# Performance work log

Measured on AMD Instinct MI355X. Metric: run time of the kernel, lower is better.

## Reference

```python
import jax, jax.numpy as jnp
import numpy as np

G = 128   # long_term_attn_g
H = 8     # num_attn_heads


def setup_inputs() -> dict:
    key = jax.random.key(0)
    ks = jax.random.split(key, 8)
    b, d, t, dk = 8, 1024, 8192, 512  # dk = model_dim // 2
    return {
        "qk": jax.random.normal(ks[0], (b, d, t), jnp.float32),
        "masks": jnp.ones((b, 1, t), jnp.float32),
        "wq": jax.random.normal(ks[1], (dk, d), jnp.float32) * 0.02,
        "bq": jnp.zeros((dk,), jnp.float32),
        "wk": jax.random.normal(ks[2], (dk, d), jnp.float32) * 0.02,
        "bk": jnp.zeros((dk,), jnp.float32),
        "wv": jax.random.normal(ks[3], (dk, d), jnp.float32) * 0.02,
        "bv": jnp.zeros((dk,), jnp.float32),
        "wo": jax.random.normal(ks[4], (d, dk), jnp.float32) * 0.02,
        "bo": jnp.zeros((d,), jnp.float32),
    }


def _to_patches(x, g):
    # convert_to_patches + rearrange 'b d np p -> (b p) d np'
    b, d, t = x.shape
    pad = (-t) % g
    x = jnp.pad(x, ((0, 0), (0, 0), (0, pad)))
    npat = x.shape[-1] // g
    return x.reshape(b, d, npat, g).transpose(0, 3, 1, 2).reshape(b * g, d, npat)


def reference(qk, masks, wq, bq, wk, bk, wv, bv, wo, bo):
    b, d, t = qk.shape
    xp = _to_patches(qk, G)     # [(b g), d, npat]  -- q, k, v source
    mp = _to_patches(masks, G)  # [(b g), 1, npat]  -- key-side attention mask

    # pointwise Conv1d projections == per-timestep matmuls
    q = jnp.einsum('od,bdt->bot', wq, xp) + bq[:, None]
    k = jnp.einsum('od,bdt->bot', wk, xp) + bk[:, None]
    v = jnp.einsum('od,bdt->bot', wv, xp) + bv[:, None]

    dk = wq.shape[0]
    dh = dk // H
    bg, _, npat = q.shape
    qh = q.reshape(bg, H, dh, npat)
    kh = k.reshape(bg, H, dh, npat)
    vh = v.reshape(bg, H, dh, npat)

    scores = jnp.einsum('bhdi,bhdj->bhij', qh, kh) / jnp.sqrt(jnp.float32(dh))
    scores = jnp.where(mp[:, :, None, :] > 0, scores, jnp.float32(-1e9))
    attn = jax.nn.softmax(scores, axis=-1)
    out = jnp.einsum('bhij,bhdj->bhdi', attn, vh).reshape(bg, dk, npat)

    # out_proj = GELU -> Conv1d(dk -> model_dim, k=1)
    out = jax.nn.gelu(out, approximate=False)
    out = jnp.einsum('od,bdt->bot', wo, out) + bo[:, None]

    # undo reshape: '(b g) d np -> b d (np g)', trim padding
    out = out.reshape(b, G, d, npat).transpose(0, 2, 3, 1).reshape(b, d, npat * G)[:, :, :t]
    return out * masks
```

## Files before the change

kernel.cpp:

```cpp
#include <hip/hip_runtime.h>
#include <hip/hip_bf16.h>
#include <cmath>

typedef __attribute__((ext_vector_type(4))) float f32x4;
typedef __attribute__((ext_vector_type(8))) short s16x8;

typedef __attribute__((address_space(1))) const void glb_void_t;
typedef __attribute__((address_space(3))) void lds_void_t;

#define MFMA(a, b, c) __builtin_amdgcn_mfma_f32_16x16x32_bf16(a, b, c, 0, 0, 0)
#define GLOAD_LDS(g, l) __builtin_amdgcn_global_load_lds((glb_void_t*)(g), (lds_void_t*)(l), 16, 0, 0)

__device__ __forceinline__ unsigned short bf(float x) {
  union { float f; unsigned u; } c; c.f = x;
  unsigned r = (c.u + 0x7fffu + ((c.u >> 16) & 1u)) >> 16;
  return (unsigned short)r;
}

__global__ void k_prep(const float* __restrict__ wq, const float* __restrict__ wk,
                       const float* __restrict__ wv, const float* __restrict__ bq,
                       const float* __restrict__ bk, const float* __restrict__ bv,
                       const float* __restrict__ wo,
                       __hip_bfloat16* __restrict__ wqkv, __hip_bfloat16* __restrict__ wob,
                       float* __restrict__ bqkv) {
  const int NW = 1536 * 1024, NO = 1024 * 512;
  for (int i = blockIdx.x * blockDim.x + threadIdx.x; i < NW + NO + 1536;
       i += gridDim.x * blockDim.x) {
    if (i < NW) {
      int r = i >> 10;
      float v = (r < 512) ? wq[i] : ((r < 1024) ? wk[i - 512 * 1024] : wv[i - 1024 * 1024]);
      ((unsigned short*)wqkv)[i] = bf(v);
    } else if (i < NW + NO) {
      int j = i - NW;
      ((unsigned short*)wob)[j] = bf(wo[j]);
    } else {
      int j = i - NW - NO;
      bqkv[j] = (j < 512) ? bq[j] : ((j < 1024) ? bk[j - 512] : bv[j - 1024]);
    }
  }
}

__global__ __launch_bounds__(256) void k_transpose(const float* __restrict__ qk,
                                                   __hip_bfloat16* __restrict__ qkT) {
  __shared__ float tile[64][65];
  const int b = blockIdx.z, t0 = blockIdx.x * 64, d0 = blockIdx.y * 64;
  const int tid = threadIdx.x;
  const int tq = tid & 15, dr = tid >> 4;
  const float* src = qk + ((size_t)b * 1024 + d0) * 8192 + t0;
#pragma unroll
  for (int i = 0; i < 4; i++) {
    int d = dr + i * 16;
    float4 v = *(const float4*)(src + (size_t)d * 8192 + tq * 4);
    tile[d][tq * 4 + 0] = v.x; tile[d][tq * 4 + 1] = v.y;
    tile[d][tq * 4 + 2] = v.z; tile[d][tq * 4 + 3] = v.w;
  }
  __syncthreads();
  const int d4 = (tid & 15) * 4, tr = tid >> 4;
  unsigned short* dst = (unsigned short*)qkT + ((size_t)b * 8192 + t0) * 1024 + d0;
#pragma unroll
  for (int i = 0; i < 4; i++) {
    int t = tr + i * 16;
    ushort4 o4;
    o4.x = bf(tile[d4 + 0][t]); o4.y = bf(tile[d4 + 1][t]);
    o4.z = bf(tile[d4 + 2][t]); o4.w = bf(tile[d4 + 3][t]);
    *(ushort4*)(dst + (size_t)t * 1024 + d4) = o4;
  }
}

__device__ __forceinline__ void stage_half(char* lds_base, const char* gbase,
                                           int ktile, int w, int l) {
#pragma unroll
  for (int r = 0; r < 2; ++r) {
    int row = r * 64 + w * 8 + (l >> 3);
    int cb = ((l & 7) * 16) ^ ((row & 7) << 4);
    GLOAD_LDS(gbase + (size_t)row * 2048 + (size_t)ktile * 128 + cb,
              lds_base + (r * 64 + w * 8) * 128);
  }
}

__global__ __launch_bounds__(512, 2) void k_qkv(const __hip_bfloat16* __restrict__ qkT,
                                                const __hip_bfloat16* __restrict__ wqkv,
                                                const float* __restrict__ bqkv,
                                                __hip_bfloat16* __restrict__ qkv) {
  __shared__ char smem[131072];
  const int NT = 16;
  const int b = blockIdx.z, t0 = blockIdx.x * 256, o0 = blockIdx.y * 256;
  const int tid = threadIdx.x, l = tid & 63, w = tid >> 6;
  const int c = l & 15, g = l >> 4;
  const int wm = w >> 2, wn = w & 3;
  const int cbase = (g * 16) ^ ((c & 7) << 4);

  const char* qpanel = (const char*)qkT + ((size_t)b * 8192 + t0) * 2048;
  const char* wpanel = (const char*)wqkv + (size_t)o0 * 2048;

#define STAGE_A(tt, h) stage_half(smem + ((tt)&1) * 32768 + (h) * 16384, \
                                  qpanel + (size_t)(h) * 262144, (tt), w, l)
#define STAGE_B(tt, h) stage_half(smem + 65536 + ((tt)&1) * 32768 + (h) * 16384, \
                                  wpanel + (size_t)(h) * 262144, (tt), w, l)

  f32x4 acc[8][4];
#pragma unroll
  for (int i = 0; i < 8; i++)
#pragma unroll
    for (int j = 0; j < 4; j++) acc[i][j] = (f32x4){0.f, 0.f, 0.f, 0.f};

  STAGE_A(0, 0); STAGE_A(0, 1); STAGE_B(0, 0); STAGE_B(0, 1);
  STAGE_B(1, 0); STAGE_A(1, 0); STAGE_A(1, 1);
  asm volatile("s_waitcnt vmcnt(6)" ::: "memory");
  __builtin_amdgcn_s_barrier();

#pragma unroll 2
  for (int t = 0; t < NT; ++t) {
    const int buf = t & 1;
    const char* Ah = smem + buf * 32768 + wm * 16384;
    const char* Bh = smem + 65536 + buf * 32768 + (wn >> 1) * 16384;
    const int brow = (wn & 1) * 64;
    s16x8 avLo[4][2], avHi[4][2], bv[4][2];

#pragma unroll
    for (int mi = 0; mi < 4; ++mi)
#pragma unroll
      for (int kk = 0; kk < 2; ++kk)
        avLo[mi][kk] = *(const s16x8*)(Ah + (mi * 16 + c) * 128 + (cbase ^ (kk << 6)));
#pragma unroll
    for (int ni = 0; ni < 4; ++ni)
#pragma unroll
      for (int kk = 0; kk < 2; ++kk)
        bv[ni][kk] = *(const s16x8*)(Bh + (brow + ni * 16 + c) * 128 + (cbase ^ (kk << 6)));
    if (t + 1 < NT) STAGE_B(t + 1, 1);
    __builtin_amdgcn_s_barrier();
    asm volatile("s_waitcnt lgkmcnt(0)" ::: "memory");
    __builtin_amdgcn_sched_barrier(0);
    __builtin_amdgcn_s_setprio(1);
#pragma unroll
    for (int mi = 0; mi < 4; ++mi)
#pragma unroll
      for (int ni = 0; ni < 2; ++ni)
#pragma unroll
        for (int kk = 0; kk < 2; ++kk)
          acc[mi][ni] = MFMA(avLo[mi][kk], bv[ni][kk], acc[mi][ni]);
    __builtin_amdgcn_s_setprio(0);
    __builtin_amdgcn_s_barrier();

#pragma unroll
    for (int mi = 0; mi < 4; ++mi)
#pragma unroll
      for (int kk = 0; kk < 2; ++kk)
        avHi[mi][kk] = *(const s16x8*)(Ah + (64 + mi * 16 + c) * 128 + (cbase ^ (kk << 6)));
    if (t + 2 < NT) STAGE_B(t + 2, 0);
    __builtin_amdgcn_s_barrier();
    asm volatile("s_waitcnt lgkmcnt(0)" ::: "memory");
    __builtin_amdgcn_sched_barrier(0);
    __builtin_amdgcn_s_setprio(1);
#pragma unroll
    for (int mi = 0; mi < 4; ++mi)
#pragma unroll
      for (int ni = 0; ni < 2; ++ni)
#pragma unroll
        for (int kk = 0; kk < 2; ++kk)
          acc[mi][ni + 2] = MFMA(avLo[mi][kk], bv[ni + 2][kk], acc[mi][ni + 2]);
    __builtin_amdgcn_s_setprio(0);
    __builtin_amdgcn_s_barrier();

    if (t + 2 < NT) STAGE_A(t + 2, 0);
    __builtin_amdgcn_s_barrier();
    __builtin_amdgcn_s_setprio(1);
#pragma unroll
    for (int mi = 0; mi < 4; ++mi)
#pragma unroll
      for (int ni = 0; ni < 2; ++ni)
#pragma unroll
        for (int kk = 0; kk < 2; ++kk)
          acc[mi + 4][ni] = MFMA(avHi[mi][kk], bv[ni][kk], acc[mi + 4][ni]);
    __builtin_amdgcn_s_setprio(0);
    __builtin_amdgcn_s_barrier();

    if (t + 2 < NT) STAGE_A(t + 2, 1);
    if (t + 2 < NT) {
      asm volatile("s_waitcnt vmcnt(6)" ::: "memory");
    } else {
      asm volatile("s_waitcnt vmcnt(0)" ::: "memory");
    }
    __builtin_amdgcn_s_barrier();
    __builtin_amdgcn_sched_barrier(0);
    __builtin_amdgcn_s_setprio(1);
#pragma unroll
    for (int mi = 0; mi < 4; ++mi)
#pragma unroll
      for (int ni = 0; ni < 2; ++ni)
#pragma unroll
        for (int kk = 0; kk < 2; ++kk)
          acc[mi + 4][ni + 2] = MFMA(avHi[mi][kk], bv[ni + 2][kk], acc[mi + 4][ni + 2]);
    __builtin_amdgcn_s_setprio(0);
    __builtin_amdgcn_s_barrier();
  }
#undef STAGE_A
#undef STAGE_B

  unsigned short* outb = (unsigned short*)qkv + ((size_t)b * 8192 + t0) * 1536 + o0;
  float bias[4];
#pragma unroll
  for (int ni = 0; ni < 4; ni++) bias[ni] = bqkv[o0 + wn * 64 + ni * 16 + c];
#pragma unroll
  for (int mi = 0; mi < 8; mi++)
#pragma unroll
    for (int r = 0; r < 4; r++) {
      int t = wm * 128 + mi * 16 + g * 4 + r;
#pragma unroll
      for (int ni = 0; ni < 4; ni++) {
        int o = wn * 64 + ni * 16 + c;
        outb[(size_t)t * 1536 + o] = bf(acc[mi][ni][r] + bias[ni]);
      }
    }
}

__global__ __launch_bounds__(64) void k_attn(const __hip_bfloat16* __restrict__ qkv,
                                             const float* __restrict__ masks,
                                             __hip_bfloat16* __restrict__ a_out) {
  const int l = threadIdx.x, c = l & 15, g = l >> 4;
  const int h = blockIdx.x & 7, bg = blockIdx.x >> 3;
  const int gg = bg & 127, b = bg >> 7;
  const size_t rowstep = (size_t)128 * 1536;
  const __hip_bfloat16* base = qkv + ((size_t)b * 8192 + gg) * 1536 + h * 64;
  const __hip_bfloat16* Qb = base;
  const __hip_bfloat16* Kb = base + 512;
  const __hip_bfloat16* Vb = base + 1024;

  s16x8 kf[4][2], qf[4][2];
#pragma unroll
  for (int f = 0; f < 4; f++)
#pragma unroll
    for (int kk = 0; kk < 2; kk++) {
      size_t roff = (size_t)(f * 16 + c) * rowstep + kk * 32 + g * 8;
      kf[f][kk] = *(const s16x8*)(Kb + roff);
      qf[f][kk] = *(const s16x8*)(Qb + roff);
    }
  f32x4 st[4][4];
#pragma unroll
  for (int i = 0; i < 4; i++)
#pragma unroll
    for (int j = 0; j < 4; j++) st[i][j] = (f32x4){0.f, 0.f, 0.f, 0.f};
#pragma unroll
  for (int mj = 0; mj < 4; mj++)
#pragma unroll
    for (int ni = 0; ni < 4; ni++)
#pragma unroll
      for (int kk = 0; kk < 2; kk++)
        st[mj][ni] = MFMA(kf[mj][kk], qf[ni][kk], st[mj][ni]);

  float mk[4][4];
#pragma unroll
  for (int mj = 0; mj < 4; mj++)
#pragma unroll
    for (int r = 0; r < 4; r++)
      mk[mj][r] = masks[(size_t)b * 8192 + (size_t)(mj * 16 + g * 4 + r) * 128 + gg];

  float inv[4];
#pragma unroll
  for (int ni = 0; ni < 4; ni++) {
    float m = -1e30f;
#pragma unroll
    for (int mj = 0; mj < 4; mj++)
#pragma unroll
      for (int r = 0; r < 4; r++) {
        float s = st[mj][ni][r] * 0.125f;
        s = (mk[mj][r] > 0.f) ? s : -1e9f;
        st[mj][ni][r] = s;
        m = fmaxf(m, s);
      }
    m = fmaxf(m, __shfl_xor(m, 16));
    m = fmaxf(m, __shfl_xor(m, 32));
    float sm = 0.f;
#pragma unroll
    for (int mj = 0; mj < 4; mj++)
#pragma unroll
      for (int r = 0; r < 4; r++) {
        float p = expf(st[mj][ni][r] - m);
        st[mj][ni][r] = p;
        sm += p;
      }
    sm += __shfl_xor(sm, 16);
    sm += __shfl_xor(sm, 32);
    inv[ni] = 1.f / sm;
  }
#pragma unroll
  for (int mj = 0; mj < 4; mj++)
#pragma unroll
    for (int ni = 0; ni < 4; ni++)
#pragma unroll
      for (int r = 0; r < 4; r++) st[mj][ni][r] *= inv[ni];

  unsigned qd[4][4][2];
#pragma unroll
  for (int ni = 0; ni < 4; ni++)
#pragma unroll
    for (int mj = 0; mj < 4; mj++)
#pragma unroll
      for (int wv = 0; wv < 2; wv++)
        qd[ni][mj][wv] = (unsigned)bf(st[mj][ni][2 * wv]) |
                         ((unsigned)bf(st[mj][ni][2 * wv + 1]) << 16);

  f32x4 oacc[4][4];
#pragma unroll
  for (int i = 0; i < 4; i++)
#pragma unroll
    for (int j = 0; j < 4; j++) oacc[i][j] = (f32x4){0.f, 0.f, 0.f, 0.f};

  const int srcA = c + 32 * (g & 1);
  const int srcB = srcA + 16;
  const bool hi = (g >= 2);
#pragma unroll
  for (int kk = 0; kk < 2; kk++) {
    s16x8 af[4];
#pragma unroll
    for (int ni = 0; ni < 4; ni++) {
      unsigned a0 = __shfl(qd[ni][2 * kk][0], srcA);
      unsigned b0 = __shfl(qd[ni][2 * kk + 1][0], srcA);
      unsigned a1 = __shfl(qd[ni][2 * kk][1], srcA);
      unsigned b1 = __shfl(qd[ni][2 * kk + 1][1], srcA);
      unsigned a2 = __shfl(qd[ni][2 * kk][0], srcB);
      unsigned b2 = __shfl(qd[ni][2 * kk + 1][0], srcB);
      unsigned a3 = __shfl(qd[ni][2 * kk][1], srcB);
      unsigned b3 = __shfl(qd[ni][2 * kk + 1][1], srcB);
      union { unsigned u[4]; s16x8 v; } uu;
      uu.u[0] = hi ? b0 : a0;
      uu.u[1] = hi ? b1 : a1;
      uu.u[2] = hi ? b2 : a2;
      uu.u[3] = hi ? b3 : a3;
      af[ni] = uu.v;
    }
    s16x8 bvv[4];
#pragma unroll
    for (int fd = 0; fd < 4; fd++) {
      s16x8 t;
#pragma unroll
      for (int e = 0; e < 8; e++)
        t[e] = *(const short*)(Vb + (size_t)(kk * 32 + g * 8 + e) * rowstep + fd * 16 + c);
      bvv[fd] = t;
    }
#pragma unroll
    for (int fi = 0; fi < 4; fi++)
#pragma unroll
      for (int fd = 0; fd < 4; fd++)
        oacc[fi][fd] = MFMA(af[fi], bvv[fd], oacc[fi][fd]);
  }

  unsigned short* ob = (unsigned short*)a_out + ((size_t)b * 8192 + gg) * 512 + h * 64;
#pragma unroll
  for (int fi = 0; fi < 4; fi++)
#pragma unroll
    for (int fd = 0; fd < 4; fd++)
#pragma unroll
      for (int r = 0; r < 4; r++) {
        float x = oacc[fi][fd][r];
        float ge = 0.5f * x * (1.f + erff(x * 0.70710678118f));
        int i = fi * 16 + g * 4 + r;
        ob[(size_t)i * (128 * 512) + fd * 16 + c] = bf(ge);
      }
}

__global__ __launch_bounds__(512) void k_out(const __hip_bfloat16* __restrict__ wob,
                                             const __hip_bfloat16* __restrict__ a,
                                             const float* __restrict__ bo,
                                             const float* __restrict__ masks,
                                             float* __restrict__ y) {
  __shared__ char smem[256 * 128 + 128 * 128];
  char* As = smem;
  char* Bs = smem + 32768;
  const int b = blockIdx.z, t0 = blockIdx.x * 128, o0 = blockIdx.y * 256;
  const int tid = threadIdx.x, l = tid & 63, w = tid >> 6;
  const int c = l & 15, g = l >> 4;
  const int wm = w >> 1, wn = w & 1;
  const int lrow = l >> 3, lcol = (l & 7) * 16;

  f32x4 acc[4][4];
#pragma unroll
  for (int i = 0; i < 4; i++)
#pragma unroll
    for (int j = 0; j < 4; j++) acc[i][j] = (f32x4){0.f, 0.f, 0.f, 0.f};

  const char* wbase = (const char*)(wob + (size_t)o0 * 512);
  const char* abase = (const char*)(a + ((size_t)b * 8192 + t0) * 512);

  for (int ks = 0; ks < 8; ks++) {
    __syncthreads();
#pragma unroll
    for (int ii = 0; ii < 4; ii++) {
      int row = w * 32 + ii * 8 + lrow;
      int cb = lcol ^ ((row & 7) << 4);
      const char* gp = wbase + (size_t)row * 1024 + ks * 128 + cb;
      GLOAD_LDS(gp, As + (w * 32 + ii * 8) * 128);
    }
#pragma unroll
    for (int ii = 0; ii < 2; ii++) {
      int row = w * 16 + ii * 8 + lrow;
      int cb = lcol ^ ((row & 7) << 4);
      const char* gp = abase + (size_t)row * 1024 + ks * 128 + cb;
      GLOAD_LDS(gp, Bs + (w * 16 + ii * 8) * 128);
    }
    __syncthreads();
#pragma unroll
    for (int kk = 0; kk < 2; kk++) {
      s16x8 av[4], bv[4];
#pragma unroll
      for (int mi = 0; mi < 4; mi++) {
        int row = wm * 64 + mi * 16 + c;
        int cb = (kk * 64 + g * 16) ^ ((row & 7) << 4);
        av[mi] = *(const s16x8*)(As + row * 128 + cb);
      }
#pragma unroll
      for (int ni = 0; ni < 4; ni++) {
        int row = wn * 64 + ni * 16 + c;
        int cb = (kk * 64 + g * 16) ^ ((row & 7) << 4);
        bv[ni] = *(const s16x8*)(Bs + row * 128 + cb);
      }
#pragma unroll
      for (int mi = 0; mi < 4; mi++)
#pragma unroll
        for (int ni = 0; ni < 4; ni++)
          acc[mi][ni] = MFMA(av[mi], bv[ni], acc[mi][ni]);
    }
  }
  int tcol[4];
  float mk[4];
#pragma unroll
  for (int ni = 0; ni < 4; ni++) {
    tcol[ni] = t0 + wn * 64 + ni * 16 + c;
    mk[ni] = masks[(size_t)b * 8192 + tcol[ni]];
  }
#pragma unroll
  for (int mi = 0; mi < 4; mi++)
#pragma unroll
    for (int r = 0; r < 4; r++) {
      int od = o0 + wm * 64 + mi * 16 + g * 4 + r;
      float bias = bo[od];
      float* yrow = y + ((size_t)b * 1024 + od) * 8192;
#pragma unroll
      for (int ni = 0; ni < 4; ni++)
        yrow[tcol[ni]] = (acc[mi][ni][r] + bias) * mk[ni];
    }
}

extern "C" void kernel_launch(void* const* d_in, const int* in_sizes, int n_in,
                              void* d_out, int out_size, void* d_ws, size_t ws_size,
                              hipStream_t stream) {
  const float* qk = (const float*)d_in[0];
  const float* masks = (const float*)d_in[1];
  const float* wq = (const float*)d_in[2];
  const float* bq = (const float*)d_in[3];
  const float* wk = (const float*)d_in[4];
  const float* bk = (const float*)d_in[5];
  const float* wv = (const float*)d_in[6];
  const float* bv = (const float*)d_in[7];
  const float* wo = (const float*)d_in[8];
  const float* bo = (const float*)d_in[9];

  char* ws = (char*)d_ws;
  __hip_bfloat16* qkT = (__hip_bfloat16*)ws;
  __hip_bfloat16* a = (__hip_bfloat16*)ws;
  __hip_bfloat16* wqkv = (__hip_bfloat16*)(ws + 134217728);
  __hip_bfloat16* wob = (__hip_bfloat16*)(ws + 134217728 + 3145728);
  float* bqkv = (float*)(ws + 134217728 + 3145728 + 1048576);

  __hip_bfloat16* qkv = (__hip_bfloat16*)d_out;
  float* y = (float*)d_out;

  k_prep<<<dim3(512), dim3(256), 0, stream>>>(wq, wk, wv, bq, bk, bv, wo, wqkv, wob, bqkv);
  k_transpose<<<dim3(128, 16, 8), dim3(256), 0, stream>>>(qk, qkT);
  k_qkv<<<dim3(32, 6, 8), dim3(512), 0, stream>>>(qkT, wqkv, bqkv, qkv);
  k_attn<<<dim3(8192), dim3(64), 0, stream>>>(qkv, masks, a);
  k_out<<<dim3(64, 4, 8), dim3(512), 0, stream>>>(wob, a, bo, masks, y);
}
```

Baseline: 470.6 us.

## Software-pipeline LDS fragment loads across iterations in QKV GEMM

Restructures the QKV projection GEMM main loop so the next tile's A-low and B-low fragments are read from LDS during the last MFMA phase of the current iteration, and splits the remaining fragment reads across phases with partial lgkmcnt waits. Global-to-LDS staging is regrouped into whole-tile A and B stages issued at two points per iteration instead of four half-stages. The goal is to hide LDS read latency behind MFMA work and reduce stalls at barriers. It raises register pressure from the carried fragments, and the hand-tuned waitcnt counts must exactly match the number of outstanding loads.

New measurement: 471.8 us. About the same (+0.2%).

```diff
diff --git a/kernel.cpp b/kernel.cpp
--- a/kernel.cpp
+++ b/kernel.cpp
@@ -89,14 +89,15 @@
   const int c = l & 15, g = l >> 4;
   const int wm = w >> 2, wn = w & 3;
   const int cbase = (g * 16) ^ ((c & 7) << 4);
+  const int brow = (wn & 1) * 64;
 
   const char* qpanel = (const char*)qkT + ((size_t)b * 8192 + t0) * 2048;
   const char* wpanel = (const char*)wqkv + (size_t)o0 * 2048;
 
-#define STAGE_A(tt, h) stage_half(smem + ((tt)&1) * 32768 + (h) * 16384, \
-                                  qpanel + (size_t)(h) * 262144, (tt), w, l)
-#define STAGE_B(tt, h) stage_half(smem + 65536 + ((tt)&1) * 32768 + (h) * 16384, \
-                                  wpanel + (size_t)(h) * 262144, (tt), w, l)
+#define STAGE_B2(tt) { stage_half(smem + 65536 + ((tt)&1) * 32768, wpanel, (tt), w, l); \
+                       stage_half(smem + 65536 + ((tt)&1) * 32768 + 16384, wpanel + 262144, (tt), w, l); }
+#define STAGE_A2(tt) { stage_half(smem + ((tt)&1) * 32768, qpanel, (tt), w, l); \
+                       stage_half(smem + ((tt)&1) * 32768 + 16384, qpanel + 262144, (tt), w, l); }
 
   f32x4 acc[8][4];
 #pragma unroll
@@ -104,30 +105,79 @@
 #pragma unroll
     for (int j = 0; j < 4; j++) acc[i][j] = (f32x4){0.f, 0.f, 0.f, 0.f};
 
-  STAGE_A(0, 0); STAGE_A(0, 1); STAGE_B(0, 0); STAGE_B(0, 1);
-  STAGE_B(1, 0); STAGE_A(1, 0); STAGE_A(1, 1);
-  asm volatile("s_waitcnt vmcnt(6)" ::: "memory");
+  STAGE_B2(0); STAGE_A2(0); STAGE_B2(1); STAGE_A2(1);
+  asm volatile("s_waitcnt vmcnt(8)" ::: "memory");
   __builtin_amdgcn_s_barrier();
+  __builtin_amdgcn_sched_barrier(0);
+
+  s16x8 avLo[4][2], avHi[4][2], bvLo[2][2], bvHi[2][2];
+  {
+    const char* Ah = smem + wm * 16384;
+    const char* Bh = smem + 65536 + (wn >> 1) * 16384;
+#pragma unroll
+    for (int mi = 0; mi < 4; ++mi)
+#pragma unroll
+      for (int kk = 0; kk < 2; ++kk)
+        avLo[mi][kk] = *(const s16x8*)(Ah + (mi * 16 + c) * 128 + (cbase ^ (kk << 6)));
+#pragma unroll
+    for (int ni = 0; ni < 2; ++ni)
+#pragma unroll
+      for (int kk = 0; kk < 2; ++kk)
+        bvLo[ni][kk] = *(const s16x8*)(Bh + (brow + ni * 16 + c) * 128 + (cbase ^ (kk << 6)));
+  }
 
 #pragma unroll 2
   for (int t = 0; t < NT; ++t) {
     const int buf = t & 1;
     const char* Ah = smem + buf * 32768 + wm * 16384;
     const char* Bh = smem + 65536 + buf * 32768 + (wn >> 1) * 16384;
-    const int brow = (wn & 1) * 64;
-    s16x8 avLo[4][2], avHi[4][2], bv[4][2];
-
+    const char* Ah2 = smem + (buf ^ 1) * 32768 + wm * 16384;
+    const char* Bh2 = smem + 65536 + (buf ^ 1) * 32768 + (wn >> 1) * 16384;
+
+#pragma unroll
+    for (int ni = 0; ni < 2; ++ni)
+#pragma unroll
+      for (int kk = 0; kk < 2; ++kk)
+        bvHi[ni][kk] = *(const s16x8*)(Bh + (brow + (2 + ni) * 16 + c) * 128 + (cbase ^ (kk << 6)));
+#pragma unroll
+    for (int mi = 0; mi < 2; ++mi)
+#pragma unroll
+      for (int kk = 0; kk < 2; ++kk)
+        avHi[mi][kk] = *(const s16x8*)(Ah + (64 + mi * 16 + c) * 128 + (cbase ^ (kk << 6)));
+    __builtin_amdgcn_s_barrier();
+    asm volatile("s_waitcnt lgkmcnt(8)" ::: "memory");
+    __builtin_amdgcn_sched_barrier(0);
+    __builtin_amdgcn_s_setprio(1);
 #pragma unroll
     for (int mi = 0; mi < 4; ++mi)
 #pragma unroll
+      for (int ni = 0; ni < 2; ++ni)
+#pragma unroll
+        for (int kk = 0; kk < 2; ++kk)
+          acc[mi][ni] = MFMA(avLo[mi][kk], bvLo[ni][kk], acc[mi][ni]);
+    __builtin_amdgcn_s_setprio(0);
+    __builtin_amdgcn_s_barrier();
+
+#pragma unroll
+    for (int mi = 2; mi < 4; ++mi)
+#pragma unroll
       for (int kk = 0; kk < 2; ++kk)
-        avLo[mi][kk] = *(const s16x8*)(Ah + (mi * 16 + c) * 128 + (cbase ^ (kk << 6)));
-#pragma unroll
-    for (int ni = 0; ni < 4; ++ni)
-#pragma unroll
-      for (int kk = 0; kk < 2; ++kk)
-        bv[ni][kk] = *(const s16x8*)(Bh + (brow + ni * 16 + c) * 128 + (cbase ^ (kk << 6)));
-    if (t + 1 < NT) STAGE_B(t + 1, 1);
+        avHi[mi][kk] = *(const s16x8*)(Ah + (64 + mi * 16 + c) * 128 + (cbase ^ (kk << 6)));
+    __builtin_amdgcn_s_barrier();
+    asm volatile("s_waitcnt lgkmcnt(8)" ::: "memory");
+    __builtin_amdgcn_sched_barrier(0);
+    __builtin_amdgcn_s_setprio(1);
+#pragma unroll
+    for (int mi = 0; mi < 4; ++mi)
+#pragma unroll
+      for (int ni = 0; ni < 2; ++ni)
+#pragma unroll
+        for (int kk = 0; kk < 2; ++kk)
+          acc[mi][ni + 2] = MFMA(avLo[mi][kk], bvHi[ni][kk], acc[mi][ni + 2]);
+    __builtin_amdgcn_s_setprio(0);
+    __builtin_amdgcn_s_barrier();
+
+    if (t + 2 < NT) STAGE_B2(t + 2);
     __builtin_amdgcn_s_barrier();
     asm volatile("s_waitcnt lgkmcnt(0)" ::: "memory");
     __builtin_amdgcn_sched_barrier(0);
@@ -138,51 +188,30 @@
       for (int ni = 0; ni < 2; ++ni)
 #pragma unroll
         for (int kk = 0; kk < 2; ++kk)
-          acc[mi][ni] = MFMA(avLo[mi][kk], bv[ni][kk], acc[mi][ni]);
+          acc[mi + 4][ni] = MFMA(avHi[mi][kk], bvLo[ni][kk], acc[mi + 4][ni]);
     __builtin_amdgcn_s_setprio(0);
     __builtin_amdgcn_s_barrier();
 
-#pragma unroll
-    for (int mi = 0; mi < 4; ++mi)
-#pragma unroll
-      for (int kk = 0; kk < 2; ++kk)
-        avHi[mi][kk] = *(const s16x8*)(Ah + (64 + mi * 16 + c) * 128 + (cbase ^ (kk << 6)));
-    if (t + 2 < NT) STAGE_B(t + 2, 0);
-    __builtin_amdgcn_s_barrier();
-    asm volatile("s_waitcnt lgkmcnt(0)" ::: "memory");
-    __builtin_amdgcn_sched_barrier(0);
-    __builtin_amdgcn_s_setprio(1);
-#pragma unroll
-    for (int mi = 0; mi < 4; ++mi)
-#pragma unroll
-      for (int ni = 0; ni < 2; ++ni)
-#pragma unroll
-        for (int kk = 0; kk < 2; ++kk)
-          acc[mi][ni + 2] = MFMA(avLo[mi][kk], bv[ni + 2][kk], acc[mi][ni + 2]);
-    __builtin_amdgcn_s_setprio(0);
-    __builtin_amdgcn_s_barrier();
-
-    if (t + 2 < NT) STAGE_A(t + 2, 0);
-    __builtin_amdgcn_s_barrier();
-    __builtin_amdgcn_s_setprio(1);
-#pragma unroll
-    for (int mi = 0; mi < 4; ++mi)
-#pragma unroll
-      for (int ni = 0; ni < 2; ++ni)
-#pragma unroll
-        for (int kk = 0; kk < 2; ++kk)
-          acc[mi + 4][ni] = MFMA(avHi[mi][kk], bv[ni][kk], acc[mi + 4][ni]);
-    __builtin_amdgcn_s_setprio(0);
-    __builtin_amdgcn_s_barrier();
-
-    if (t + 2 < NT) STAGE_A(t + 2, 1);
+    if (t + 2 < NT) STAGE_A2(t + 2);
     if (t + 2 < NT) {
-      asm volatile("s_waitcnt vmcnt(6)" ::: "memory");
+      asm volatile("s_waitcnt vmcnt(8)" ::: "memory");
     } else {
       asm volatile("s_waitcnt vmcnt(0)" ::: "memory");
     }
     __builtin_amdgcn_s_barrier();
     __builtin_amdgcn_sched_barrier(0);
+    if (t + 1 < NT) {
+#pragma unroll
+      for (int mi = 0; mi < 4; ++mi)
+#pragma unroll
+        for (int kk = 0; kk < 2; ++kk)
+          avLo[mi][kk] = *(const s16x8*)(Ah2 + (mi * 16 + c) * 128 + (cbase ^ (kk << 6)));
+#pragma unroll
+      for (int ni = 0; ni < 2; ++ni)
+#pragma unroll
+        for (int kk = 0; kk < 2; ++kk)
+          bvLo[ni][kk] = *(const s16x8*)(Bh2 + (brow + ni * 16 + c) * 128 + (cbase ^ (kk << 6)));
+    }
     __builtin_amdgcn_s_setprio(1);
 #pragma unroll
     for (int mi = 0; mi < 4; ++mi)
@@ -190,12 +219,12 @@
       for (int ni = 0; ni < 2; ++ni)
 #pragma unroll
         for (int kk = 0; kk < 2; ++kk)
-          acc[mi + 4][ni + 2] = MFMA(avHi[mi][kk], bv[ni + 2][kk], acc[mi + 4][ni + 2]);
+          acc[mi + 4][ni + 2] = MFMA(avHi[mi][kk], bvHi[ni][kk], acc[mi + 4][ni + 2]);
     __builtin_amdgcn_s_setprio(0);
     __builtin_amdgcn_s_barrier();
   }
-#undef STAGE_A
-#undef STAGE_B
+#undef STAGE_A2
+#undef STAGE_B2
 
   unsigned short* outb = (unsigned short*)qkv + ((size_t)b * 8192 + t0) * 1536 + o0;
   float bias[4];
```

## Restructure QKV GEMM pipeline with split B fragments and reordered A/B staging

Applied to the files above, without the earlier changes.

Reworks the k_qkv main loop schedule. B fragments are now read in two halves, and global-to-LDS staging is reordered: A is prefetched one tile ahead into the other buffer while B is prefetched two tiles ahead, with adjusted vmcnt/lgkmcnt waits. The launch bounds drop the min-blocks-per-CU hint of 2, which lets the compiler use more registers. The aim is better overlap of loads with MFMA and fewer register-pressure constraints, at the risk of lower occupancy and subtle buffer hazards.

After: 466.0 us. Within noise of the previous version (-1.0%).

```diff
diff --git a/kernel.cpp b/kernel.cpp
--- a/kernel.cpp
+++ b/kernel.cpp
@@ -78,10 +78,10 @@
   }
 }
 
-__global__ __launch_bounds__(512, 2) void k_qkv(const __hip_bfloat16* __restrict__ qkT,
-                                                const __hip_bfloat16* __restrict__ wqkv,
-                                                const float* __restrict__ bqkv,
-                                                __hip_bfloat16* __restrict__ qkv) {
+__global__ __launch_bounds__(512) void k_qkv(const __hip_bfloat16* __restrict__ qkT,
+                                             const __hip_bfloat16* __restrict__ wqkv,
+                                             const float* __restrict__ bqkv,
+                                             __hip_bfloat16* __restrict__ qkv) {
   __shared__ char smem[131072];
   const int NT = 16;
   const int b = blockIdx.z, t0 = blockIdx.x * 256, o0 = blockIdx.y * 256;
@@ -89,14 +89,16 @@
   const int c = l & 15, g = l >> 4;
   const int wm = w >> 2, wn = w & 3;
   const int cbase = (g * 16) ^ ((c & 7) << 4);
+  const int brow = (wn & 1) * 64;
 
   const char* qpanel = (const char*)qkT + ((size_t)b * 8192 + t0) * 2048;
   const char* wpanel = (const char*)wqkv + (size_t)o0 * 2048;
 
-#define STAGE_A(tt, h) stage_half(smem + ((tt)&1) * 32768 + (h) * 16384, \
-                                  qpanel + (size_t)(h) * 262144, (tt), w, l)
-#define STAGE_B(tt, h) stage_half(smem + 65536 + ((tt)&1) * 32768 + (h) * 16384, \
-                                  wpanel + (size_t)(h) * 262144, (tt), w, l)
+#define STG_A(PAR, h, tt) stage_half(smem + (PAR) * 32768 + (h) * 16384, \
+                                     qpanel + (size_t)(h) * 262144, (tt), w, l)
+#define STG_B(PAR, h, tt) stage_half(smem + 65536 + (PAR) * 32768 + (h) * 16384, \
+                                     wpanel + (size_t)(h) * 262144, (tt), w, l)
+#define RD(base, row, kk) (*(const s16x8*)((base) + (row) * 128 + (cbase ^ ((kk) << 6))))
 
   f32x4 acc[8][4];
 #pragma unroll
@@ -104,98 +106,90 @@
 #pragma unroll
     for (int j = 0; j < 4; j++) acc[i][j] = (f32x4){0.f, 0.f, 0.f, 0.f};
 
-  STAGE_A(0, 0); STAGE_A(0, 1); STAGE_B(0, 0); STAGE_B(0, 1);
-  STAGE_B(1, 0); STAGE_A(1, 0); STAGE_A(1, 1);
-  asm volatile("s_waitcnt vmcnt(6)" ::: "memory");
+  STG_A(0, 0, 0); STG_A(0, 1, 0); STG_B(0, 0, 0); STG_B(0, 1, 0);
+  STG_B(1, 0, 1); STG_B(1, 1, 1);
+  asm volatile("s_waitcnt vmcnt(4)" ::: "memory");
   __builtin_amdgcn_s_barrier();
 
-#pragma unroll 2
+#define QUAD(AV, BV, AOFF, NOFF)                                          \
+  _Pragma("unroll") for (int mi = 0; mi < 4; ++mi)                        \
+  _Pragma("unroll") for (int ni = 0; ni < 2; ++ni)                        \
+  _Pragma("unroll") for (int kk = 0; kk < 2; ++kk)                        \
+    acc[mi + AOFF][ni + NOFF] = MFMA(AV[mi][kk], BV[ni][kk], acc[mi + AOFF][ni + NOFF]);
+
   for (int t = 0; t < NT; ++t) {
-    const int buf = t & 1;
-    const char* Ah = smem + buf * 32768 + wm * 16384;
-    const char* Bh = smem + 65536 + buf * 32768 + (wn >> 1) * 16384;
-    const int brow = (wn & 1) * 64;
-    s16x8 avLo[4][2], avHi[4][2], bv[4][2];
+    const int PAR = t & 1;
+    const char* Ab = smem + PAR * 32768 + wm * 16384;
+    const char* Bb = smem + 65536 + PAR * 32768 + (wn >> 1) * 16384;
+    const bool doA = (t + 1 < NT);
+    const bool doB = (t + 2 < NT);
+    s16x8 avLo[4][2], avHi[4][2], bvLo[2][2], bvHi[2][2];
 
 #pragma unroll
     for (int mi = 0; mi < 4; ++mi)
 #pragma unroll
       for (int kk = 0; kk < 2; ++kk)
-        avLo[mi][kk] = *(const s16x8*)(Ah + (mi * 16 + c) * 128 + (cbase ^ (kk << 6)));
-#pragma unroll
-    for (int ni = 0; ni < 4; ++ni)
+        avLo[mi][kk] = RD(Ab, mi * 16 + c, kk);
+#pragma unroll
+    for (int ni = 0; ni < 2; ++ni)
 #pragma unroll
       for (int kk = 0; kk < 2; ++kk)
-        bv[ni][kk] = *(const s16x8*)(Bh + (brow + ni * 16 + c) * 128 + (cbase ^ (kk << 6)));
-    if (t + 1 < NT) STAGE_B(t + 1, 1);
+        bvLo[ni][kk] = RD(Bb, brow + ni * 16 + c, kk);
+    if (doA) STG_A(PAR ^ 1, 0, t + 1);
+    asm volatile("s_waitcnt lgkmcnt(8)" ::: "memory");
     __builtin_amdgcn_s_barrier();
     asm volatile("s_waitcnt lgkmcnt(0)" ::: "memory");
     __builtin_amdgcn_sched_barrier(0);
     __builtin_amdgcn_s_setprio(1);
-#pragma unroll
-    for (int mi = 0; mi < 4; ++mi)
-#pragma unroll
-      for (int ni = 0; ni < 2; ++ni)
-#pragma unroll
-        for (int kk = 0; kk < 2; ++kk)
-          acc[mi][ni] = MFMA(avLo[mi][kk], bv[ni][kk], acc[mi][ni]);
+    QUAD(avLo, bvLo, 0, 0);
     __builtin_amdgcn_s_setprio(0);
     __builtin_amdgcn_s_barrier();
 
 #pragma unroll
-    for (int mi = 0; mi < 4; ++mi)
+    for (int ni = 0; ni < 2; ++ni)
 #pragma unroll
       for (int kk = 0; kk < 2; ++kk)
-        avHi[mi][kk] = *(const s16x8*)(Ah + (64 + mi * 16 + c) * 128 + (cbase ^ (kk << 6)));
-    if (t + 2 < NT) STAGE_B(t + 2, 0);
+        bvHi[ni][kk] = RD(Bb, brow + 32 + ni * 16 + c, kk);
+    if (doA) STG_A(PAR ^ 1, 1, t + 1);
     __builtin_amdgcn_s_barrier();
     asm volatile("s_waitcnt lgkmcnt(0)" ::: "memory");
     __builtin_amdgcn_sched_barrier(0);
     __builtin_amdgcn_s_setprio(1);
+    QUAD(avLo, bvHi, 0, 2);
+    __builtin_amdgcn_s_setprio(0);
+    __builtin_amdgcn_s_barrier();
+
 #pragma unroll
     for (int mi = 0; mi < 4; ++mi)
 #pragma unroll
-      for (int ni = 0; ni < 2; ++ni)
-#pragma unroll
-        for (int kk = 0; kk < 2; ++kk)
-          acc[mi][ni + 2] = MFMA(avLo[mi][kk], bv[ni + 2][kk], acc[mi][ni + 2]);
+      for (int kk = 0; kk < 2; ++kk)
+        avHi[mi][kk] = RD(Ab, 64 + mi * 16 + c, kk);
+    if (doB) STG_B(PAR, 0, t + 2);
+    __builtin_amdgcn_s_barrier();
+    asm volatile("s_waitcnt lgkmcnt(0)" ::: "memory");
+    __builtin_amdgcn_sched_barrier(0);
+    __builtin_amdgcn_s_setprio(1);
+    QUAD(avHi, bvLo, 4, 0);
     __builtin_amdgcn_s_setprio(0);
     __builtin_amdgcn_s_barrier();
 
-    if (t + 2 < NT) STAGE_A(t + 2, 0);
-    __builtin_amdgcn_s_barrier();
-    __builtin_amdgcn_s_setprio(1);
-#pragma unroll
-    for (int mi = 0; mi < 4; ++mi)
-#pragma unroll
-      for (int ni = 0; ni < 2; ++ni)
-#pragma unroll
-        for (int kk = 0; kk < 2; ++kk)
-          acc[mi + 4][ni] = MFMA(avHi[mi][kk], bv[ni][kk], acc[mi + 4][ni]);
-    __builtin_amdgcn_s_setprio(0);
-    __builtin_amdgcn_s_barrier();
-
-    if (t + 2 < NT) STAGE_A(t + 2, 1);
-    if (t + 2 < NT) {
-      asm volatile("s_waitcnt vmcnt(6)" ::: "memory");
+    if (doB) STG_B(PAR, 1, t + 2);
+    if (t < NT - 2) {
+      asm volatile("s_waitcnt vmcnt(4)" ::: "memory");
     } else {
       asm volatile("s_waitcnt vmcnt(0)" ::: "memory");
     }
     __builtin_amdgcn_s_barrier();
     __builtin_amdgcn_sched_barrier(0);
     __builtin_amdgcn_s_setprio(1);
-#pragma unroll
-    for (int mi = 0; mi < 4; ++mi)
-#pragma unroll
-      for (int ni = 0; ni < 2; ++ni)
-#pragma unroll
-        for (int kk = 0; kk < 2; ++kk)
-          acc[mi + 4][ni + 2] = MFMA(avHi[mi][kk], bv[ni + 2][kk], acc[mi + 4][ni + 2]);
+    QUAD(avHi, bvHi, 4, 2);
     __builtin_amdgcn_s_setprio(0);
     __builtin_amdgcn_s_barrier();
   }
-#undef STAGE_A
-#undef STAGE_B
+#undef QUAD
+#undef RD
+#undef STG_A
+#undef STG_B
 
   unsigned short* outb = (unsigned short*)qkv + ((size_t)b * 8192 + t0) * 1536 + o0;
   float bias[4];
```
